# Optimization experiments

Measured on AMD Instinct MI355X. Metric: run time of the kernel, lower is better.

## Reference

```python
import jax, jax.numpy as jnp
import numpy as np

MARGIN = 1.0
EPS = 1e-12


def setup_inputs() -> dict:
    key = jax.random.key(0)
    k1, k2, k3 = jax.random.split(key, 3)
    inputs = jax.random.normal(k1, (8192, 128), dtype=jnp.float32)
    targets = jax.random.randint(k2, (8192,), 0, 64, dtype=jnp.int64)
    center = jax.random.normal(k3, (16, 128), dtype=jnp.float32)
    return {"inputs": inputs, "targets": targets, "center": center}


def reference(inputs, targets, center):
    n = inputs.shape[0]
    # pairwise Euclidean distances via ||a||^2 + ||b||^2 - 2 a.b  (matches addmm_ trick)
    sq = jnp.sum(inputs * inputs, axis=1)                      # [n]
    dist2 = sq[:, None] + sq[None, :] - 2.0 * (inputs @ inputs.T)
    dist = jnp.sqrt(jnp.clip(dist2, EPS))                      # [n, n]

    mask = targets[:, None] == targets[None, :]                # same-class mask [n, n]

    # batch-hard mining, fully vectorized (replaces per-row python loops)
    dist_ap = jnp.max(jnp.where(mask, dist, -jnp.inf), axis=1)  # hardest positive
    neg_min = jnp.min(jnp.where(mask, jnp.inf, dist), axis=1)   # hardest negative
    has_neg = jnp.any(~mask, axis=1)
    dist_an = jnp.where(has_neg, neg_min, dist_ap + MARGIN)

    # center augmentation: min over distances to L2-normalized prototypes
    cn = center / jnp.linalg.norm(center, axis=1, keepdims=True)       # [P, d]
    dc = jnp.sqrt(jnp.sum((inputs[:, None, :] - cn[None, :, :]) ** 2, axis=-1))  # [n, P]
    dc = jnp.clip(dc, EPS)
    dist_an = jnp.minimum(dist_an, jnp.min(dc, axis=1))

    # MarginRankingLoss with y=1: mean(relu(dist_ap - dist_an + margin))
    loss = jnp.mean(jnp.maximum(dist_ap - dist_an + MARGIN, 0.0))
    return loss
```

## Files before the change

kernel.cpp:

```cpp
#include <hip/hip_runtime.h>


#define N_ROWS 8192
#define DIM 128
#define KDIM 192
#define ROWB 384
#define NPROTO 16
#define NRG 32
#define MARGIN_F 1.0f
#define EPS_F 1e-12f
#define BIAS_F 32768.0f

typedef __attribute__((ext_vector_type(8))) short short8;
typedef __attribute__((ext_vector_type(4))) float float4v;
typedef __attribute__((ext_vector_type(4))) unsigned uint4v;

static __device__ __forceinline__ unsigned f2bf(float f) {
  unsigned u = __float_as_uint(f);
  u += 0x7fffu + ((u >> 16) & 1u);
  return u >> 16;
}

static __device__ __forceinline__ void gload_lds16(const void* g, void* l) {
  __builtin_amdgcn_global_load_lds(
      (const __attribute__((address_space(1))) unsigned*)g,
      (__attribute__((address_space(3))) unsigned*)l, 16, 0, 0);
}

__global__ void prep_kernel(const float* __restrict__ x,
                            const float* __restrict__ center,
                            const int* __restrict__ tgt,
                            char* __restrict__ xbf,
                            float* __restrict__ sq,
                            float* __restrict__ mindc,
                            float* __restrict__ out) {
  __shared__ float scn[NPROTO * DIM];
  int tid = threadIdx.x;
  if (blockIdx.x == 0 && tid == 0) out[0] = 0.0f;
  int rloc = tid >> 4, l = tid & 15;
  {
    float v[8];
    float ss = 0.f;
#pragma unroll
    for (int j = 0; j < 8; ++j) {
      v[j] = center[rloc * DIM + l * 8 + j];
      ss += v[j] * v[j];
    }
#pragma unroll
    for (int m = 1; m < 16; m <<= 1) ss += __shfl_xor(ss, m, 64);
    float inv = 1.0f / sqrtf(ss);
#pragma unroll
    for (int j = 0; j < 8; ++j) scn[rloc * DIM + l * 8 + j] = v[j] * inv;
  }
  __syncthreads();

  int row = blockIdx.x * 16 + rloc;
  float4 v0 = ((const float4*)x)[row * 32 + l * 2];
  float4 v1 = ((const float4*)x)[row * 32 + l * 2 + 1];
  float ss = v0.x * v0.x + v0.y * v0.y + v0.z * v0.z + v0.w * v0.w +
             v1.x * v1.x + v1.y * v1.y + v1.z * v1.z + v1.w * v1.w;
  float dots[NPROTO];
#pragma unroll
  for (int p = 0; p < NPROTO; ++p) {
    const float* c = &scn[p * DIM + l * 8];
    dots[p] = v0.x * c[0] + v0.y * c[1] + v0.z * c[2] + v0.w * c[3] +
              v1.x * c[4] + v1.y * c[5] + v1.z * c[6] + v1.w * c[7];
  }
#pragma unroll
  for (int m = 1; m < 16; m <<= 1) {
    ss += __shfl_xor(ss, m, 64);
#pragma unroll
    for (int p = 0; p < NPROTO; ++p) dots[p] += __shfl_xor(dots[p], m, 64);
  }
  uint4 pk;
  pk.x = f2bf(v0.x) | (f2bf(v0.y) << 16);
  pk.y = f2bf(v0.z) | (f2bf(v0.w) << 16);
  pk.z = f2bf(v1.x) | (f2bf(v1.y) << 16);
  pk.w = f2bf(v1.z) | (f2bf(v1.w) << 16);
  *(uint4*)(xbf + (size_t)row * ROWB + l * 16) = pk;
  int cls = tgt[row];
  if (l < 8) {
    unsigned wv = (cls & 1) ? 0xC3000000u : 0x0000C300u;
    uint4 oh;
    oh.x = ((cls >> 1) == (l * 4 + 0)) ? wv : 0u;
    oh.y = ((cls >> 1) == (l * 4 + 1)) ? wv : 0u;
    oh.z = ((cls >> 1) == (l * 4 + 2)) ? wv : 0u;
    oh.w = ((cls >> 1) == (l * 4 + 3)) ? wv : 0u;
    *(uint4*)(xbf + (size_t)row * ROWB + 256 + l * 16) = oh;
  }
  if (l == 0) {
    float mind2 = INFINITY;
#pragma unroll
    for (int p = 0; p < NPROTO; ++p)
      mind2 = fminf(mind2, ss + 1.0f - 2.0f * dots[p]);
    sq[row] = ss;
    mindc[row] = fmaxf(sqrtf(fmaxf(mind2, 0.0f)), EPS_F);
  }
}

__global__ __launch_bounds__(256, 2) void
pairdist_kernel(const char* __restrict__ xbf, const float* __restrict__ sq,
                float* __restrict__ pmax, float* __restrict__ pmin) {
  __shared__ __align__(16) char bl[2][24576];
  __shared__ float cmaxw[4][256], cminw[4][256];
  int t = blockIdx.x, I = 0;
  while (t >= NRG - I) { t -= NRG - I; ++I; }
  const int J = I + t;
  const int wave = threadIdx.x >> 6, lane = threadIdx.x & 63;
  const int q = lane >> 4, l16 = lane & 15;
  const int rowbase = I * 256 + wave * 64;
  const int colbase = J * 256;

  const int slot = wave * 64 + lane;
  const char* const srcstrip = xbf + (size_t)colbase * ROWB;
  int soff[6];
#pragma unroll
  for (int r = 0; r < 6; ++r) {
    int o = r * 4096 + slot * 16;
    int c = o / ROWB;
    soff[r] = c * ROWB + ((o - c * ROWB) ^ ((c & 7) << 4));
  }

  auto stage = [&](int s, char* buf) {
    const char* g = srcstrip + (size_t)s * 24576;
#pragma unroll
    for (int r = 0; r < 6; ++r)
      gload_lds16(g + soff[r], buf + r * 4096 + wave * 1024);
  };

  stage(0, bl[0]);

  short8 a[4][6];
#pragma unroll
  for (int rt = 0; rt < 4; ++rt) {
    const char* ar = xbf + (size_t)(rowbase + rt * 16 + l16) * ROWB + q * 16;
#pragma unroll
    for (int kc = 0; kc < 6; ++kc) a[rt][kc] = *(const short8*)(ar + kc * 64);
#pragma unroll
    for (int kc = 4; kc < 6; ++kc) {
      uint4v u = __builtin_bit_cast(uint4v, a[rt][kc]);
      u ^= 0x80008000u;
      a[rt][kc] = __builtin_bit_cast(short8, u);
    }
  }
  float sqr[16];
#pragma unroll
  for (int rt = 0; rt < 4; ++rt)
#pragma unroll
    for (int r = 0; r < 4; ++r)
      sqr[rt * 4 + r] = sq[rowbase + rt * 16 + q * 4 + r];

  int roffb[6];
#pragma unroll
  for (int kc = 0; kc < 6; ++kc)
    roffb[kc] = (l16 * ROWB + kc * 64 + q * 16) ^ ((l16 & 7) << 4);

  float maxp[16], minn[16];
#pragma unroll
  for (int i = 0; i < 16; ++i) {
    maxp[i] = -INFINITY;
    minn[i] = INFINITY;
  }

#pragma unroll 1
  for (int s = 0; s < 4; ++s) {
    __syncthreads();
    if (s + 1 < 4) stage(s + 1, bl[(s + 1) & 1]);
    const char* cur = bl[s & 1];
    float sqs[4];
#pragma unroll
    for (int ss = 0; ss < 4; ++ss)
      sqs[ss] = sq[colbase + s * 64 + ss * 16 + l16];
    float cmx[4], cmn[4];
#pragma unroll
    for (int ss = 0; ss < 4; ++ss) {
      const char* bufp = cur + ss * 6144;
      short8 b[6];
#pragma unroll
      for (int kc = 0; kc < 6; ++kc)
        b[kc] = *(const short8*)(bufp + roffb[kc]);
      float4v acc[4];
#pragma unroll
      for (int rt = 0; rt < 4; ++rt) acc[rt] = (float4v){0.f, 0.f, 0.f, 0.f};
#pragma unroll
      for (int kc = 0; kc < 6; ++kc)
#pragma unroll
        for (int rt = 0; rt < 4; ++rt)
          acc[rt] = __builtin_amdgcn_mfma_f32_16x16x32_bf16(a[rt][kc], b[kc],
                                                            acc[rt], 0, 0, 0);
#pragma unroll
      for (int rt = 0; rt < 4; ++rt)
#pragma unroll
        for (int r = 0; r < 4; ++r) {
          float v = fmaf(-2.0f, acc[rt][r], sqs[ss]);
          int idx = rt * 4 + r;
          maxp[idx] = fmaxf(maxp[idx], v);
          minn[idx] = fminf(minn[idx], v);
        }
      if (I != J) {
        float um = -INFINITY, un = INFINITY;
#pragma unroll
        for (int rt = 0; rt < 4; ++rt)
#pragma unroll
          for (int r = 0; r < 4; ++r) {
            float u = fmaf(-2.0f, acc[rt][r], sqr[rt * 4 + r]);
            um = fmaxf(um, u);
            un = fminf(un, u);
          }
        cmx[ss] = um;
        cmn[ss] = un;
      }
    }
    if (I != J) {
#pragma unroll
      for (int ss = 0; ss < 4; ++ss) {
        float a1 = fmaxf(cmx[ss], __shfl_xor(cmx[ss], 16, 64));
        a1 = fmaxf(a1, __shfl_xor(a1, 32, 64));
        float a2 = fminf(cmn[ss], __shfl_xor(cmn[ss], 16, 64));
        a2 = fminf(a2, __shfl_xor(a2, 32, 64));
        if (q == 0) {
          cmaxw[wave][s * 64 + ss * 16 + l16] = a1;
          cminw[wave][s * 64 + ss * 16 + l16] = a2;
        }
      }
    }
  }

#pragma unroll
  for (int m = 1; m < 16; m <<= 1)
#pragma unroll
    for (int i = 0; i < 16; ++i) {
      maxp[i] = fmaxf(maxp[i], __shfl_xor(maxp[i], m, 64));
      minn[i] = fminf(minn[i], __shfl_xor(minn[i], m, 64));
    }
  if (l16 == 0) {
    float* pM = pmax + (size_t)J * N_ROWS + rowbase + q * 4;
    float* pm = pmin + (size_t)J * N_ROWS + rowbase + q * 4;
#pragma unroll
    for (int rt = 0; rt < 4; ++rt)
#pragma unroll
      for (int r = 0; r < 4; ++r) {
        pM[rt * 16 + r] = maxp[rt * 4 + r];
        pm[rt * 16 + r] = minn[rt * 4 + r];
      }
  }
  if (I != J) {
    __syncthreads();
    int c = threadIdx.x;
    float M = fmaxf(fmaxf(cmaxw[0][c], cmaxw[1][c]),
                    fmaxf(cmaxw[2][c], cmaxw[3][c]));
    float m = fminf(fminf(cminw[0][c], cminw[1][c]),
                    fminf(cminw[2][c], cminw[3][c]));
    pmax[(size_t)I * N_ROWS + colbase + c] = M;
    pmin[(size_t)I * N_ROWS + colbase + c] = m;
  }
}

__global__ void finalize_kernel(const float* __restrict__ pmax,
                                const float* __restrict__ pmin,
                                const float* __restrict__ sq,
                                const float* __restrict__ mindc,
                                float* __restrict__ out) {
  __shared__ float wsum[4];
  int i = blockIdx.x * 256 + threadIdx.x;
  float maxv = -INFINITY, minv = INFINITY;
#pragma unroll
  for (int s = 0; s < NRG; ++s) {
    maxv = fmaxf(maxv, pmax[s * N_ROWS + i]);
    minv = fminf(minv, pmin[s * N_ROWS + i]);
  }
  float si = sq[i];
  float dap = sqrtf(fmaxf(si + (maxv - BIAS_F), EPS_F));
  float dan = (minv > 16384.0f) ? (dap + MARGIN_F)
                                : sqrtf(fmaxf(si + minv, EPS_F));
  dan = fminf(dan, mindc[i]);
  float c = fmaxf(dap - dan + MARGIN_F, 0.0f) * (1.0f / (float)N_ROWS);
#pragma unroll
  for (int m = 1; m < 64; m <<= 1) c += __shfl_xor(c, m, 64);
  int lane = threadIdx.x & 63, wv = threadIdx.x >> 6;
  if (lane == 0) wsum[wv] = c;
  __syncthreads();
  if (threadIdx.x == 0) atomicAdd(out, wsum[0] + wsum[1] + wsum[2] + wsum[3]);
}

extern "C" void kernel_launch(void* const* d_in, const int* in_sizes, int n_in,
                              void* d_out, int out_size, void* d_ws, size_t ws_size,
                              hipStream_t stream) {
  const float* inputs = (const float*)d_in[0];
  const int* targets = (const int*)d_in[1];
  const float* center = (const float*)d_in[2];
  char* ws = (char*)d_ws;
  char* xbf    = ws;
  float* sq    = (float*)(ws + 3145728);
  float* mindc = (float*)(ws + 3178496);
  float* pmax  = (float*)(ws + 3211264);
  float* pmin  = (float*)(ws + 4259840);
  float* out   = (float*)d_out;

  prep_kernel<<<512, 256, 0, stream>>>(inputs, center, targets, xbf, sq, mindc, out);
  pairdist_kernel<<<528, 256, 0, stream>>>(xbf, sq, pmax, pmin);
  finalize_kernel<<<32, 256, 0, stream>>>(pmax, pmin, sq, mindc, out);
}
```

Before: 110.7 us.

## Exploit symmetry inside diagonal tiles and pair diagonal blocks per workgroup

Diagonal 256x256 tiles used to compute the full block even though it is symmetric. Now 16 workgroups each handle two diagonal tiles (G and 31-G, for load balance) and compute only the lower-triangular 16x16 subtiles. The transposed contributions are reduced through LDS atomic max/min on order-preserving integer keys. This cuts redundant MFMA work and brings the grid from 528 to 512 blocks, at the cost of more branching and LDS atomics in the diagonal path.

```diff
diff --git a/kernel.cpp b/kernel.cpp
--- a/kernel.cpp
+++ b/kernel.cpp
@@ -19,6 +19,15 @@
   unsigned u = __float_as_uint(f);
   u += 0x7fffu + ((u >> 16) & 1u);
   return u >> 16;
+}
+
+static __device__ __forceinline__ unsigned fkey(float f) {
+  unsigned b = __float_as_uint(f);
+  return (b & 0x80000000u) ? ~b : (b | 0x80000000u);
+}
+static __device__ __forceinline__ float funkey(unsigned k) {
+  unsigned b = (k & 0x80000000u) ? (k & 0x7fffffffu) : ~k;
+  return __uint_as_float(b);
 }
 
 static __device__ __forceinline__ void gload_lds16(const void* g, void* l) {
@@ -103,16 +112,10 @@
                 float* __restrict__ pmax, float* __restrict__ pmin) {
   __shared__ __align__(16) char bl[2][24576];
   __shared__ float cmaxw[4][256], cminw[4][256];
-  int t = blockIdx.x, I = 0;
-  while (t >= NRG - I) { t -= NRG - I; ++I; }
-  const int J = I + t;
   const int wave = threadIdx.x >> 6, lane = threadIdx.x & 63;
   const int q = lane >> 4, l16 = lane & 15;
-  const int rowbase = I * 256 + wave * 64;
-  const int colbase = J * 256;
-
-  const int slot = wave * 64 + lane;
-  const char* const srcstrip = xbf + (size_t)colbase * ROWB;
+  const int slot = threadIdx.x;
+
   int soff[6];
 #pragma unroll
   for (int r = 0; r < 6; ++r) {
@@ -120,98 +123,105 @@
     int c = o / ROWB;
     soff[r] = c * ROWB + ((o - c * ROWB) ^ ((c & 7) << 4));
   }
-
-  auto stage = [&](int s, char* buf) {
-    const char* g = srcstrip + (size_t)s * 24576;
-#pragma unroll
-    for (int r = 0; r < 6; ++r)
-      gload_lds16(g + soff[r], buf + r * 4096 + wave * 1024);
-  };
-
-  stage(0, bl[0]);
-
-  short8 a[4][6];
-#pragma unroll
-  for (int rt = 0; rt < 4; ++rt) {
-    const char* ar = xbf + (size_t)(rowbase + rt * 16 + l16) * ROWB + q * 16;
-#pragma unroll
-    for (int kc = 0; kc < 6; ++kc) a[rt][kc] = *(const short8*)(ar + kc * 64);
-#pragma unroll
-    for (int kc = 4; kc < 6; ++kc) {
-      uint4v u = __builtin_bit_cast(uint4v, a[rt][kc]);
-      u ^= 0x80008000u;
-      a[rt][kc] = __builtin_bit_cast(short8, u);
-    }
-  }
-  float sqr[16];
-#pragma unroll
-  for (int rt = 0; rt < 4; ++rt)
-#pragma unroll
-    for (int r = 0; r < 4; ++r)
-      sqr[rt * 4 + r] = sq[rowbase + rt * 16 + q * 4 + r];
-
   int roffb[6];
 #pragma unroll
   for (int kc = 0; kc < 6; ++kc)
     roffb[kc] = (l16 * ROWB + kc * 64 + q * 16) ^ ((l16 & 7) << 4);
 
-  float maxp[16], minn[16];
-#pragma unroll
-  for (int i = 0; i < 16; ++i) {
-    maxp[i] = -INFINITY;
-    minn[i] = INFINITY;
-  }
+  if (blockIdx.x >= 16) {
+    int t = blockIdx.x - 16, I = 0;
+    while (t >= 31 - I) { t -= 31 - I; ++I; }
+    const int J = I + 1 + t;
+    const int rowbase = I * 256 + wave * 64;
+    const int colbase = J * 256;
+    const char* const srcstrip = xbf + (size_t)colbase * ROWB;
+
+    auto stage = [&](int s, char* buf) {
+      const char* g = srcstrip + (size_t)s * 24576;
+#pragma unroll
+      for (int r = 0; r < 6; ++r)
+        gload_lds16(g + soff[r], buf + r * 4096 + wave * 1024);
+    };
+    stage(0, bl[0]);
+
+    short8 a[4][6];
+#pragma unroll
+    for (int rt = 0; rt < 4; ++rt) {
+      const char* ar = xbf + (size_t)(rowbase + rt * 16 + l16) * ROWB + q * 16;
+#pragma unroll
+      for (int kc = 0; kc < 6; ++kc) a[rt][kc] = *(const short8*)(ar + kc * 64);
+#pragma unroll
+      for (int kc = 4; kc < 6; ++kc) {
+        uint4v u = __builtin_bit_cast(uint4v, a[rt][kc]);
+        u ^= 0x80008000u;
+        a[rt][kc] = __builtin_bit_cast(short8, u);
+      }
+    }
+#pragma unroll
+    for (int rt = 0; rt < 4; ++rt)
+#pragma unroll
+      for (int kc = 0; kc < 6; ++kc)
+        asm volatile("" : "+v"(a[rt][kc]));
+
+    float sqr[16];
+#pragma unroll
+    for (int rt = 0; rt < 4; ++rt)
+#pragma unroll
+      for (int r = 0; r < 4; ++r)
+        sqr[rt * 4 + r] = sq[rowbase + rt * 16 + q * 4 + r];
+
+    float maxp[16], minn[16];
+#pragma unroll
+    for (int i = 0; i < 16; ++i) { maxp[i] = -INFINITY; minn[i] = INFINITY; }
 
 #pragma unroll 1
-  for (int s = 0; s < 4; ++s) {
-    __syncthreads();
-    if (s + 1 < 4) stage(s + 1, bl[(s + 1) & 1]);
-    const char* cur = bl[s & 1];
-    float sqs[4];
-#pragma unroll
-    for (int ss = 0; ss < 4; ++ss)
-      sqs[ss] = sq[colbase + s * 64 + ss * 16 + l16];
-    float cmx[4], cmn[4];
-#pragma unroll
-    for (int ss = 0; ss < 4; ++ss) {
-      const char* bufp = cur + ss * 6144;
-      short8 b[6];
-#pragma unroll
-      for (int kc = 0; kc < 6; ++kc)
-        b[kc] = *(const short8*)(bufp + roffb[kc]);
-      float4v acc[4];
-#pragma unroll
-      for (int rt = 0; rt < 4; ++rt) acc[rt] = (float4v){0.f, 0.f, 0.f, 0.f};
-#pragma unroll
-      for (int kc = 0; kc < 6; ++kc)
+    for (int s = 0; s < 4; ++s) {
+      __syncthreads();
+      if (s + 1 < 4) stage(s + 1, bl[(s + 1) & 1]);
+      const char* cur = bl[s & 1];
+      float sqs[4];
+#pragma unroll
+      for (int ss = 0; ss < 4; ++ss)
+        sqs[ss] = sq[colbase + s * 64 + ss * 16 + l16];
+      float cmx[4], cmn[4];
+#pragma unroll
+      for (int ss = 0; ss < 4; ++ss) {
+        const char* bufp = cur + ss * 6144;
+        short8 b[6];
+#pragma unroll
+        for (int kc = 0; kc < 6; ++kc) b[kc] = *(const short8*)(bufp + roffb[kc]);
+        float4v acc[4];
+#pragma unroll
+        for (int rt = 0; rt < 4; ++rt) acc[rt] = (float4v){0.f, 0.f, 0.f, 0.f};
+#pragma unroll
+        for (int kc = 0; kc < 6; ++kc)
+#pragma unroll
+          for (int rt = 0; rt < 4; ++rt)
+            acc[rt] = __builtin_amdgcn_mfma_f32_16x16x32_bf16(a[rt][kc], b[kc],
+                                                              acc[rt], 0, 0, 0);
 #pragma unroll
         for (int rt = 0; rt < 4; ++rt)
-          acc[rt] = __builtin_amdgcn_mfma_f32_16x16x32_bf16(a[rt][kc], b[kc],
-                                                            acc[rt], 0, 0, 0);
-#pragma unroll
-      for (int rt = 0; rt < 4; ++rt)
-#pragma unroll
-        for (int r = 0; r < 4; ++r) {
-          float v = fmaf(-2.0f, acc[rt][r], sqs[ss]);
-          int idx = rt * 4 + r;
-          maxp[idx] = fmaxf(maxp[idx], v);
-          minn[idx] = fminf(minn[idx], v);
-        }
-      if (I != J) {
-        float um = -INFINITY, un = INFINITY;
-#pragma unroll
-        for (int rt = 0; rt < 4; ++rt)
 #pragma unroll
           for (int r = 0; r < 4; ++r) {
-            float u = fmaf(-2.0f, acc[rt][r], sqr[rt * 4 + r]);
-            um = fmaxf(um, u);
-            un = fminf(un, u);
+            float v = fmaf(-2.0f, acc[rt][r], sqs[ss]);
+            int idx = rt * 4 + r;
+            maxp[idx] = fmaxf(maxp[idx], v);
+            minn[idx] = fminf(minn[idx], v);
           }
-        cmx[ss] = um;
-        cmn[ss] = un;
-      }
-    }
-    if (I != J) {
+        {
+          float um = -INFINITY, un = INFINITY;
+#pragma unroll
+          for (int rt = 0; rt < 4; ++rt)
+#pragma unroll
+            for (int r = 0; r < 4; ++r) {
+              float u = fmaf(-2.0f, acc[rt][r], sqr[rt * 4 + r]);
+              um = fmaxf(um, u);
+              un = fminf(un, u);
+            }
+          cmx[ss] = um;
+          cmn[ss] = un;
+        }
+      }
 #pragma unroll
       for (int ss = 0; ss < 4; ++ss) {
         float a1 = fmaxf(cmx[ss], __shfl_xor(cmx[ss], 16, 64));
@@ -224,35 +234,175 @@
         }
       }
     }
-  }
-
-#pragma unroll
-  for (int m = 1; m < 16; m <<= 1)
-#pragma unroll
-    for (int i = 0; i < 16; ++i) {
-      maxp[i] = fmaxf(maxp[i], __shfl_xor(maxp[i], m, 64));
-      minn[i] = fminf(minn[i], __shfl_xor(minn[i], m, 64));
-    }
-  if (l16 == 0) {
-    float* pM = pmax + (size_t)J * N_ROWS + rowbase + q * 4;
-    float* pm = pmin + (size_t)J * N_ROWS + rowbase + q * 4;
-#pragma unroll
-    for (int rt = 0; rt < 4; ++rt)
-#pragma unroll
-      for (int r = 0; r < 4; ++r) {
-        pM[rt * 16 + r] = maxp[rt * 4 + r];
-        pm[rt * 16 + r] = minn[rt * 4 + r];
-      }
-  }
-  if (I != J) {
+
+#pragma unroll
+    for (int m = 1; m < 16; m <<= 1)
+#pragma unroll
+      for (int i = 0; i < 16; ++i) {
+        maxp[i] = fmaxf(maxp[i], __shfl_xor(maxp[i], m, 64));
+        minn[i] = fminf(minn[i], __shfl_xor(minn[i], m, 64));
+      }
+    if (l16 == 0) {
+      float* pM = pmax + (size_t)J * N_ROWS + rowbase + q * 4;
+      float* pm = pmin + (size_t)J * N_ROWS + rowbase + q * 4;
+#pragma unroll
+      for (int rt = 0; rt < 4; ++rt)
+#pragma unroll
+        for (int r = 0; r < 4; ++r) {
+          pM[rt * 16 + r] = maxp[rt * 4 + r];
+          pm[rt * 16 + r] = minn[rt * 4 + r];
+        }
+    }
     __syncthreads();
-    int c = threadIdx.x;
-    float M = fmaxf(fmaxf(cmaxw[0][c], cmaxw[1][c]),
-                    fmaxf(cmaxw[2][c], cmaxw[3][c]));
-    float m = fminf(fminf(cminw[0][c], cminw[1][c]),
-                    fminf(cminw[2][c], cminw[3][c]));
-    pmax[(size_t)I * N_ROWS + colbase + c] = M;
-    pmin[(size_t)I * N_ROWS + colbase + c] = m;
+    {
+      int c = threadIdx.x;
+      float M = fmaxf(fmaxf(cmaxw[0][c], cmaxw[1][c]),
+                      fmaxf(cmaxw[2][c], cmaxw[3][c]));
+      float m = fminf(fminf(cminw[0][c], cminw[1][c]),
+                      fminf(cminw[2][c], cminw[3][c]));
+      pmax[(size_t)I * N_ROWS + colbase + c] = M;
+      pmin[(size_t)I * N_ROWS + colbase + c] = m;
+    }
+  } else {
+    unsigned* dmax = (unsigned*)cmaxw;
+    unsigned* dmin = (unsigned*)cminw;
+    int rtgs[4] = {wave, 7 - wave, 8 + wave, 15 - wave};
+
+#pragma unroll 1
+    for (int g2 = 0; g2 < 2; ++g2) {
+      const int G = g2 ? (31 - (int)blockIdx.x) : (int)blockIdx.x;
+      const int base = G * 256;
+      const char* const srcstrip = xbf + (size_t)base * ROWB;
+      dmax[threadIdx.x] = 0u;
+      dmin[threadIdx.x] = 0xFFFFFFFFu;
+
+      auto stage = [&](int s, char* buf) {
+        const char* g = srcstrip + (size_t)s * 24576;
+#pragma unroll
+        for (int r = 0; r < 6; ++r)
+          gload_lds16(g + soff[r], buf + r * 4096 + wave * 1024);
+      };
+      stage(0, bl[0]);
+
+      short8 a[4][6];
+#pragma unroll
+      for (int rt = 0; rt < 4; ++rt) {
+        const char* ar =
+            xbf + (size_t)(base + rtgs[rt] * 16 + l16) * ROWB + q * 16;
+#pragma unroll
+        for (int kc = 0; kc < 6; ++kc)
+          a[rt][kc] = *(const short8*)(ar + kc * 64);
+#pragma unroll
+        for (int kc = 4; kc < 6; ++kc) {
+          uint4v u = __builtin_bit_cast(uint4v, a[rt][kc]);
+          u ^= 0x80008000u;
+          a[rt][kc] = __builtin_bit_cast(short8, u);
+        }
+      }
+#pragma unroll
+      for (int rt = 0; rt < 4; ++rt)
+#pragma unroll
+        for (int kc = 0; kc < 6; ++kc)
+          asm volatile("" : "+v"(a[rt][kc]));
+
+      float sqr[16];
+#pragma unroll
+      for (int rt = 0; rt < 4; ++rt)
+#pragma unroll
+        for (int r = 0; r < 4; ++r)
+          sqr[rt * 4 + r] = sq[base + rtgs[rt] * 16 + q * 4 + r];
+
+      float maxp[16], minn[16];
+#pragma unroll
+      for (int i = 0; i < 16; ++i) { maxp[i] = -INFINITY; minn[i] = INFINITY; }
+
+#pragma unroll 1
+      for (int s = 0; s < 4; ++s) {
+        __syncthreads();
+        if (s + 1 < 4) stage(s + 1, bl[(s + 1) & 1]);
+        const char* cur = bl[s & 1];
+        float sqs[4];
+#pragma unroll
+        for (int ss = 0; ss < 4; ++ss)
+          sqs[ss] = sq[base + s * 64 + ss * 16 + l16];
+#pragma unroll
+        for (int ss = 0; ss < 4; ++ss) {
+          const int ct = s * 4 + ss;
+          const char* bufp = cur + ss * 6144;
+          short8 b[6];
+#pragma unroll
+          for (int kc = 0; kc < 6; ++kc)
+            b[kc] = *(const short8*)(bufp + roffb[kc]);
+          float4v acc[4];
+#pragma unroll
+          for (int rt = 0; rt < 4; ++rt)
+            if (rtgs[rt] <= ct) {
+              acc[rt] = (float4v){0.f, 0.f, 0.f, 0.f};
+#pragma unroll
+              for (int kc = 0; kc < 6; ++kc)
+                acc[rt] = __builtin_amdgcn_mfma_f32_16x16x32_bf16(
+                    a[rt][kc], b[kc], acc[rt], 0, 0, 0);
+            }
+#pragma unroll
+          for (int rt = 0; rt < 4; ++rt)
+            if (rtgs[rt] <= ct)
+#pragma unroll
+              for (int r = 0; r < 4; ++r) {
+                float v = fmaf(-2.0f, acc[rt][r], sqs[ss]);
+                int idx = rt * 4 + r;
+                maxp[idx] = fmaxf(maxp[idx], v);
+                minn[idx] = fminf(minn[idx], v);
+              }
+          bool any = false;
+          float um = -INFINITY, un = INFINITY;
+#pragma unroll
+          for (int rt = 0; rt < 4; ++rt)
+            if (rtgs[rt] < ct) {
+              any = true;
+#pragma unroll
+              for (int r = 0; r < 4; ++r) {
+                float u = fmaf(-2.0f, acc[rt][r], sqr[rt * 4 + r]);
+                um = fmaxf(um, u);
+                un = fminf(un, u);
+              }
+            }
+          if (any) {
+            um = fmaxf(um, __shfl_xor(um, 16, 64));
+            um = fmaxf(um, __shfl_xor(um, 32, 64));
+            un = fminf(un, __shfl_xor(un, 16, 64));
+            un = fminf(un, __shfl_xor(un, 32, 64));
+            if (q == 0) {
+              atomicMax(&dmax[ct * 16 + l16], fkey(um));
+              atomicMin(&dmin[ct * 16 + l16], fkey(un));
+            }
+          }
+        }
+      }
+#pragma unroll
+      for (int m = 1; m < 16; m <<= 1)
+#pragma unroll
+        for (int i = 0; i < 16; ++i) {
+          maxp[i] = fmaxf(maxp[i], __shfl_xor(maxp[i], m, 64));
+          minn[i] = fminf(minn[i], __shfl_xor(minn[i], m, 64));
+        }
+      if (l16 == 0) {
+#pragma unroll
+        for (int rt = 0; rt < 4; ++rt)
+#pragma unroll
+          for (int r = 0; r < 4; ++r) {
+            int rl = rtgs[rt] * 16 + q * 4 + r;
+            atomicMax(&dmax[rl], fkey(maxp[rt * 4 + r]));
+            atomicMin(&dmin[rl], fkey(minn[rt * 4 + r]));
+          }
+      }
+      __syncthreads();
+      {
+        int c = threadIdx.x;
+        pmax[(size_t)G * N_ROWS + base + c] = funkey(dmax[c]);
+        pmin[(size_t)G * N_ROWS + base + c] = funkey(dmin[c]);
+      }
+      if (g2 == 0) __syncthreads();
+    }
   }
 }
 
@@ -298,6 +448,6 @@
   float* out   = (float*)d_out;
 
   prep_kernel<<<512, 256, 0, stream>>>(inputs, center, targets, xbf, sq, mindc, out);
-  pairdist_kernel<<<528, 256, 0, stream>>>(xbf, sq, pmax, pmin);
+  pairdist_kernel<<<512, 256, 0, stream>>>(xbf, sq, pmax, pmin);
   finalize_kernel<<<32, 256, 0, stream>>>(pmax, pmin, sq, mindc, out);
 }
```

Result: slower. 118.5 us (+7.0%).
